# Kernel tuning notes

Measured on AMD Instinct MI355X. Metric: run time of the kernel, lower is better.

## Reference

```python
import jax, jax.numpy as jnp
import numpy as np

# dims per init_kwargs / input_specs
N, F_IN, H, C, L = 50000, 128, 128, 40, 4
E = 800000
ALPHA = 0.1   # args.beta -> self.alpha (initial-residual strength)
LAMDA = 0.5   # identity-mapping decay


def setup_inputs() -> dict:
    key = jax.random.key(0)
    ks = jax.random.split(key, 6)
    x = jax.random.normal(ks[0], (N, F_IN), jnp.float32)
    edge_index = jax.random.randint(ks[1], (2, E), 0, N, dtype=jnp.int32)
    s = 1.0 / np.sqrt(H)
    W_in = jax.random.uniform(ks[2], (F_IN, H), jnp.float32, -s, s)
    b_in = jnp.zeros((H,), jnp.float32)
    W_layers = jax.random.uniform(ks[3], (L, H, H), jnp.float32, -s, s)
    W_out = jax.random.uniform(ks[4], (H, C), jnp.float32, -s, s)
    b_out = jnp.zeros((C,), jnp.float32)
    return dict(x=x, edge_index=edge_index, W_in=W_in, b_in=b_in,
                W_layers=W_layers, W_out=W_out, b_out=b_out)


def _gcn_norm(edge_index, n):
    """Symmetric GCN normalization with added self-loops (gcn_norm)."""
    loops = jnp.arange(n, dtype=edge_index.dtype)
    row = jnp.concatenate([edge_index[0], loops])  # destination
    col = jnp.concatenate([edge_index[1], loops])  # source
    deg = jax.ops.segment_sum(jnp.ones(row.shape, jnp.float32), row, num_segments=n)
    dinv = jnp.where(deg > 0, jax.lax.rsqrt(jnp.maximum(deg, 1e-12)), 0.0)
    return row, col, dinv[row] * dinv[col]  # per-edge norm coefficient


def reference(x, edge_index, W_in, b_in, W_layers, W_out, b_out):
    n = x.shape[0]
    row, col, norm = _gcn_norm(edge_index, n)
    # input linear + relu (dropout is identity in eval / p=0)
    h = jax.nn.relu(x @ W_in + b_in)
    h0 = h  # _hidden[0], the initial residual
    # beta_i = log(lamda/(i+1) + 1)
    betas = jnp.log(LAMDA / jnp.arange(1, L + 1, dtype=jnp.float32) + 1.0)

    def layer(h, wb):
        W, beta = wb
        # sparse graph conv: gather-source, scale, scatter-add to dest  [E,H] msgs
        agg = jax.ops.segment_sum(h[col] * norm[:, None], row, num_segments=n)
        support = (1.0 - ALPHA) * agg + ALPHA * h0
        out = beta * (support @ W) + (1.0 - beta) * support  # ((1-b)I + bW)
        return jax.nn.relu(out), None

    h, _ = jax.lax.scan(layer, h, (W_layers, betas))
    return h @ W_out + b_out
```

## Files before the change

kernel.cpp:

```cpp
#include <hip/hip_runtime.h>
#include <hip/hip_bf16.h>
#include <hip/hip_fp16.h>
#include <math.h>

typedef short short8 __attribute__((ext_vector_type(8)));
typedef _Float16 half8 __attribute__((ext_vector_type(8)));
typedef float f32x4  __attribute__((ext_vector_type(4)));

__device__ __forceinline__ unsigned short f2bf(float f) {
    union { float f; unsigned u; } v; v.f = f;
    unsigned r = (v.u + 0x7FFFu + ((v.u >> 16) & 1u)) >> 16;
    return (unsigned short)r;
}
__device__ __forceinline__ float bf2f(unsigned short b) {
    union { unsigned u; float f; } v; v.u = ((unsigned)b) << 16; return v.f;
}
__device__ __forceinline__ unsigned short f2h(float f) {
    return __half_as_ushort(__float2half(f));
}
__device__ __forceinline__ float h2f(unsigned short u) {
    return __half2float(__ushort_as_half(u));
}


__global__ void k_count(const int* __restrict__ dst, int* __restrict__ cnt, int E) {
    int e = blockIdx.x * 256 + threadIdx.x;
    if (e < E) atomicAdd(&cnt[dst[e]], 1);
}

__global__ void k_dinv(const int* __restrict__ cnt, float* __restrict__ dinv, int n) {
    int i = blockIdx.x * 256 + threadIdx.x;
    if (i < n) dinv[i] = 1.0f / sqrtf((float)cnt[i] + 1.0f);
}

__global__ void k_scan_part(const int* __restrict__ cnt, int* __restrict__ offs,
                            int* __restrict__ parts, int n) {
    __shared__ int s[256];
    int i = blockIdx.x * 256 + threadIdx.x;
    int v = (i < n) ? cnt[i] : 0;
    s[threadIdx.x] = v;
    __syncthreads();
    #pragma unroll
    for (int d = 1; d < 256; d <<= 1) {
        int t = (threadIdx.x >= d) ? s[threadIdx.x - d] : 0;
        __syncthreads();
        s[threadIdx.x] += t;
        __syncthreads();
    }
    if (i < n) offs[i] = s[threadIdx.x] - v;
    if (threadIdx.x == 255) parts[blockIdx.x] = s[255];
}

__global__ void k_scan_tops(int* __restrict__ parts, int np) {
    __shared__ int s[256];
    int tid = threadIdx.x;
    int v = (tid < np) ? parts[tid] : 0;
    s[tid] = v;
    __syncthreads();
    #pragma unroll
    for (int d = 1; d < 256; d <<= 1) {
        int t = (tid >= d) ? s[tid - d] : 0;
        __syncthreads();
        s[tid] += t;
        __syncthreads();
    }
    if (tid < np) parts[tid] = s[tid] - v;
}

__global__ void k_scan_add(int* __restrict__ offs, const int* __restrict__ parts,
                           int n, int e_total) {
    int i = blockIdx.x * 256 + threadIdx.x;
    if (i < n) offs[i] += parts[blockIdx.x];
    if (blockIdx.x == 0 && threadIdx.x == 0) offs[n] = e_total;
}

__global__ void k_scatter(const int* __restrict__ dst, const int* __restrict__ src,
                          const int* __restrict__ offs, int* __restrict__ cur,
                          const float* __restrict__ dinv, unsigned* __restrict__ csr, int E) {
    int e = blockIdx.x * 256 + threadIdx.x;
    if (e < E) {
        int d = dst[e], s = src[e];
        int pos = offs[d] + atomicAdd(&cur[d], 1);
        float w = 0.9f * dinv[d] * dinv[s];
        unsigned hw = (unsigned)f2h(w);
        csr[pos] = (hw << 16) | (unsigned)s;
    }
}


__global__ void k_wprep(const float* __restrict__ Wl, const float* __restrict__ Win,
                        unsigned short* __restrict__ wt,
                        unsigned short* __restrict__ wht,
                        unsigned short* __restrict__ wlt) {
    int m = blockIdx.x;
    for (int i = threadIdx.x; i < 16384; i += 256) {
        int n = i >> 7, k = i & 127;
        if (m < 4) {
            wt[m * 16384 + n * 128 + k] = f2h(Wl[m * 16384 + k * 128 + n]);
        } else {
            float f = Win[k * 128 + n];
            unsigned short h = f2bf(f);
            wht[n * 128 + k] = h;
            wlt[n * 128 + k] = f2bf(f - bf2f(h));
        }
    }
}


__global__ __launch_bounds__(256)
void k_spmm(const int* __restrict__ offs, const unsigned* __restrict__ csr,
            const unsigned short* __restrict__ hb,
            const unsigned short* __restrict__ h0b,
            const float* __restrict__ dinv,
            unsigned short* __restrict__ supb, int n, int E) {
    int node = blockIdx.x * 8 + (threadIdx.x >> 5);
    if (node >= n) return;
    int l32 = threadIdx.x & 31;
    float di = dinv[node];
    float ws = 0.9f * di * di;
    uint2 sv = *(const uint2*)&hb [((size_t)node << 7) + (l32 << 2)];
    uint2 rv = *(const uint2*)&h0b[((size_t)node << 7) + (l32 << 2)];
    float ax = ws * h2f((unsigned short)(sv.x & 0xffffu)) + 0.1f * h2f((unsigned short)(rv.x & 0xffffu));
    float ay = ws * h2f((unsigned short)(sv.x >> 16))     + 0.1f * h2f((unsigned short)(rv.x >> 16));
    float az = ws * h2f((unsigned short)(sv.y & 0xffffu)) + 0.1f * h2f((unsigned short)(rv.y & 0xffffu));
    float aw = ws * h2f((unsigned short)(sv.y >> 16))     + 0.1f * h2f((unsigned short)(rv.y >> 16));
    int e = offs[node], end = offs[node + 1];
    while (e < end) {
        int nb = end - e;
        if (nb > 32) nb = 32;
        unsigned ce = csr[min(e + l32, E - 1)];
        int i = 0;
        for (; i + 8 <= nb; i += 8) {
            uint2 g[8]; float wv[8];
            #pragma unroll
            for (int j = 0; j < 8; ++j) {
                unsigned u = __shfl(ce, i + j, 32);
                wv[j] = h2f((unsigned short)(u >> 16));
                g[j] = *(const uint2*)&hb[((size_t)(u & 0xffffu) << 7) + (l32 << 2)];
            }
            #pragma unroll
            for (int j = 0; j < 8; ++j) {
                ax += wv[j] * h2f((unsigned short)(g[j].x & 0xffffu));
                ay += wv[j] * h2f((unsigned short)(g[j].x >> 16));
                az += wv[j] * h2f((unsigned short)(g[j].y & 0xffffu));
                aw += wv[j] * h2f((unsigned short)(g[j].y >> 16));
            }
        }
        for (; i + 4 <= nb; i += 4) {
            uint2 g[4]; float wv[4];
            #pragma unroll
            for (int j = 0; j < 4; ++j) {
                unsigned u = __shfl(ce, i + j, 32);
                wv[j] = h2f((unsigned short)(u >> 16));
                g[j] = *(const uint2*)&hb[((size_t)(u & 0xffffu) << 7) + (l32 << 2)];
            }
            #pragma unroll
            for (int j = 0; j < 4; ++j) {
                ax += wv[j] * h2f((unsigned short)(g[j].x & 0xffffu));
                ay += wv[j] * h2f((unsigned short)(g[j].x >> 16));
                az += wv[j] * h2f((unsigned short)(g[j].y & 0xffffu));
                aw += wv[j] * h2f((unsigned short)(g[j].y >> 16));
            }
        }
        for (; i + 2 <= nb; i += 2) {
            uint2 g[2]; float wv[2];
            #pragma unroll
            for (int j = 0; j < 2; ++j) {
                unsigned u = __shfl(ce, i + j, 32);
                wv[j] = h2f((unsigned short)(u >> 16));
                g[j] = *(const uint2*)&hb[((size_t)(u & 0xffffu) << 7) + (l32 << 2)];
            }
            #pragma unroll
            for (int j = 0; j < 2; ++j) {
                ax += wv[j] * h2f((unsigned short)(g[j].x & 0xffffu));
                ay += wv[j] * h2f((unsigned short)(g[j].x >> 16));
                az += wv[j] * h2f((unsigned short)(g[j].y & 0xffffu));
                aw += wv[j] * h2f((unsigned short)(g[j].y >> 16));
            }
        }
        for (; i < nb; ++i) {
            unsigned u = __shfl(ce, i, 32);
            float w = h2f((unsigned short)(u >> 16));
            uint2 g = *(const uint2*)&hb[((size_t)(u & 0xffffu) << 7) + (l32 << 2)];
            ax += w * h2f((unsigned short)(g.x & 0xffffu));
            ay += w * h2f((unsigned short)(g.x >> 16));
            az += w * h2f((unsigned short)(g.y & 0xffffu));
            aw += w * h2f((unsigned short)(g.y >> 16));
        }
        e += nb;
    }
    uint2 o;
    o.x = (unsigned)f2h(ax) | ((unsigned)f2h(ay) << 16);
    o.y = (unsigned)f2h(az) | ((unsigned)f2h(aw) << 16);
    *(uint2*)&supb[((size_t)node << 7) + (l32 << 2)] = o;
}


__global__ __launch_bounds__(256)
void gemm_in(const float* __restrict__ inA,
             const unsigned short* __restrict__ Bhi,
             const unsigned short* __restrict__ Blo,
             const float* __restrict__ bias,
             unsigned short* __restrict__ hb,
             unsigned short* __restrict__ h0b, int M) {
    extern __shared__ char lds[];
    char* Ahi = lds;
    char* Alo = Ahi + 8192;
    char* Whi = Alo + 8192;
    char* Wlo = Whi + 32768;

    const int tid  = threadIdx.x;
    const int row0 = blockIdx.x * 32;

    for (int c = tid; c < 512; c += 256) {
        int row = c >> 4, k8 = c & 15;
        int grow = row0 + row;
        short8 hv = {0,0,0,0,0,0,0,0};
        short8 lv = {0,0,0,0,0,0,0,0};
        if (grow < M) {
            const float* s = &inA[(size_t)grow * 128 + k8 * 8];
            float4 f0 = *(const float4*)s;
            float4 f1 = *(const float4*)(s + 4);
            float ff[8] = {f0.x, f0.y, f0.z, f0.w, f1.x, f1.y, f1.z, f1.w};
            #pragma unroll
            for (int j = 0; j < 8; ++j) {
                unsigned short hh = f2bf(ff[j]);
                hv[j] = (short)hh;
                lv[j] = (short)f2bf(ff[j] - bf2f(hh));
            }
        }
        int off = row * 256 + ((k8 ^ (row & 7)) << 4);
        *(short8*)(Ahi + off) = hv;
        *(short8*)(Alo + off) = lv;
    }
    for (int c = tid; c < 2048; c += 256) {
        int n = c >> 4, k8 = c & 15;
        int off = n * 256 + ((k8 ^ (n & 7)) << 4);
        *(short8*)(Whi + off) = *(const short8*)&Bhi[n * 128 + k8 * 8];
        *(short8*)(Wlo + off) = *(const short8*)&Blo[n * 128 + k8 * 8];
    }
    __syncthreads();

    const int lane = tid & 63;
    const int w    = tid >> 6;
    const int lr   = lane & 15;
    const int lg   = lane >> 4;

    f32x4 acc[2][2];
    #pragma unroll
    for (int m = 0; m < 2; ++m)
        #pragma unroll
        for (int n2 = 0; n2 < 2; ++n2) acc[m][n2] = (f32x4){0.f, 0.f, 0.f, 0.f};

    #pragma unroll
    for (int kk = 0; kk < 4; ++kk) {
        int k8 = kk * 4 + lg;
        short8 a[2], al[2], b[2], bl[2];
        #pragma unroll
        for (int m = 0; m < 2; ++m) {
            int row = m * 16 + lr;
            int off = row * 256 + ((k8 ^ (row & 7)) << 4);
            a[m]  = *(const short8*)(Ahi + off);
            al[m] = *(const short8*)(Alo + off);
        }
        #pragma unroll
        for (int n2 = 0; n2 < 2; ++n2) {
            int n = (w * 2 + n2) * 16 + lr;
            int off = n * 256 + ((k8 ^ (n & 7)) << 4);
            b[n2]  = *(const short8*)(Whi + off);
            bl[n2] = *(const short8*)(Wlo + off);
        }
        #pragma unroll
        for (int m = 0; m < 2; ++m)
            #pragma unroll
            for (int n2 = 0; n2 < 2; ++n2) {
                acc[m][n2] = __builtin_amdgcn_mfma_f32_16x16x32_bf16(al[m], b[n2], acc[m][n2], 0, 0, 0);
                acc[m][n2] = __builtin_amdgcn_mfma_f32_16x16x32_bf16(a[m], bl[n2], acc[m][n2], 0, 0, 0);
                acc[m][n2] = __builtin_amdgcn_mfma_f32_16x16x32_bf16(a[m], b[n2], acc[m][n2], 0, 0, 0);
            }
    }

    #pragma unroll
    for (int m = 0; m < 2; ++m) {
        #pragma unroll
        for (int n2 = 0; n2 < 2; ++n2) {
            int col = (w * 2 + n2) * 16 + lr;
            #pragma unroll
            for (int r = 0; r < 4; ++r) {
                int row = row0 + m * 16 + lg * 4 + r;
                if (row < M) {
                    float o = fmaxf(acc[m][n2][r] + bias[col], 0.f);
                    unsigned short ob = f2h(o);
                    hb [(size_t)row * 128 + col] = ob;
                    h0b[(size_t)row * 128 + col] = ob;
                }
            }
        }
    }
}


template<int LAST>
__global__ __launch_bounds__(256)
void gemm_layer(const unsigned short* __restrict__ supb,
                const unsigned short* __restrict__ Bh,
                float beta, float gamma,
                float* __restrict__ outf,
                unsigned short* __restrict__ outh, int M) {
    extern __shared__ char lds[];
    char* Ah = lds;
    char* Wh = Ah + 16384;

    const int tid  = threadIdx.x;
    const int row0 = blockIdx.x * 64;

    for (int c = tid; c < 1024; c += 256) {
        int row = c >> 4, k8 = c & 15;
        int grow = row0 + row;
        short8 hv = {0,0,0,0,0,0,0,0};
        if (grow < M) hv = *(const short8*)&supb[(size_t)grow * 128 + k8 * 8];
        *(short8*)(Ah + row * 256 + ((k8 ^ (row & 7)) << 4)) = hv;
    }
    for (int c = tid; c < 2048; c += 256) {
        int n = c >> 4, k8 = c & 15;
        *(short8*)(Wh + n * 256 + ((k8 ^ (n & 7)) << 4)) = *(const short8*)&Bh[n * 128 + k8 * 8];
    }
    __syncthreads();

    const int lane = tid & 63;
    const int w    = tid >> 6;
    const int lr   = lane & 15;
    const int lg   = lane >> 4;

    f32x4 acc[4][2];
    #pragma unroll
    for (int m = 0; m < 4; ++m)
        #pragma unroll
        for (int n2 = 0; n2 < 2; ++n2) acc[m][n2] = (f32x4){0.f, 0.f, 0.f, 0.f};

    #pragma unroll
    for (int kk = 0; kk < 4; ++kk) {
        int k8 = kk * 4 + lg;
        half8 a[4], b[2];
        #pragma unroll
        for (int m = 0; m < 4; ++m) {
            int row = m * 16 + lr;
            a[m] = *(const half8*)(Ah + row * 256 + ((k8 ^ (row & 7)) << 4));
        }
        #pragma unroll
        for (int n2 = 0; n2 < 2; ++n2) {
            int n = (w * 2 + n2) * 16 + lr;
            b[n2] = *(const half8*)(Wh + n * 256 + ((k8 ^ (n & 7)) << 4));
        }
        #pragma unroll
        for (int m = 0; m < 4; ++m)
            #pragma unroll
            for (int n2 = 0; n2 < 2; ++n2)
                acc[m][n2] = __builtin_amdgcn_mfma_f32_16x16x32_f16(a[m], b[n2], acc[m][n2], 0, 0, 0);
    }

    #pragma unroll
    for (int m = 0; m < 4; ++m) {
        #pragma unroll
        for (int n2 = 0; n2 < 2; ++n2) {
            int col = (w * 2 + n2) * 16 + lr;
            int k8c = col >> 3;
            int ebc = (col & 7) * 2;
            #pragma unroll
            for (int r = 0; r < 4; ++r) {
                int rl  = m * 16 + lg * 4 + r;
                int row = row0 + rl;
                if (row < M) {
                    unsigned short rb = *(const unsigned short*)
                        (Ah + rl * 256 + ((k8c ^ (rl & 7)) << 4) + ebc);
                    float o = beta * acc[m][n2][r] + gamma * h2f(rb);
                    o = fmaxf(o, 0.f);
                    if (LAST) outf[(size_t)row * 128 + col] = o;
                    else      outh[(size_t)row * 128 + col] = f2h(o);
                }
            }
        }
    }
}


__global__ __launch_bounds__(320)
void k_out(const float* __restrict__ h, const float* __restrict__ W,
           const float* __restrict__ b, float* __restrict__ out, int M, int C) {
    __shared__ float Ws[128 * 41];
    __shared__ float xs[32 * 132];
    const int tid  = threadIdx.x;
    const int row0 = blockIdx.x * 32;

    for (int i = tid; i < 128 * 40; i += 320) {
        int k = i / 40, c = i % 40;
        Ws[k * 41 + c] = W[i];
    }
    {
        const float4* h4 = (const float4*)h;
        for (int i = tid; i < 1024; i += 320) {
            int r = i >> 5, c4 = i & 31;
            int gr = row0 + r;
            float4 v = make_float4(0.f, 0.f, 0.f, 0.f);
            if (gr < M) v = h4[(size_t)gr * 32 + c4];
            *(float4*)&xs[r * 132 + c4 * 4] = v;
        }
    }
    __syncthreads();

    const int c  = tid % 40;
    const int rg = tid / 40;
    float acc[4] = {0.f, 0.f, 0.f, 0.f};
    #pragma unroll 4
    for (int k4 = 0; k4 < 32; ++k4) {
        float w0 = Ws[(k4 * 4 + 0) * 41 + c];
        float w1 = Ws[(k4 * 4 + 1) * 41 + c];
        float w2 = Ws[(k4 * 4 + 2) * 41 + c];
        float w3 = Ws[(k4 * 4 + 3) * 41 + c];
        #pragma unroll
        for (int i = 0; i < 4; ++i) {
            float4 x = *(const float4*)&xs[(rg * 4 + i) * 132 + k4 * 4];
            acc[i] += x.x * w0 + x.y * w1 + x.z * w2 + x.w * w3;
        }
    }
    float bb = b[c];
    #pragma unroll
    for (int i = 0; i < 4; ++i) {
        int r = row0 + rg * 4 + i;
        if (r < M) out[(size_t)r * C + c] = acc[i] + bb;
    }
}


extern "C" void kernel_launch(void* const* d_in, const int* in_sizes, int n_in,
                              void* d_out, int out_size, void* d_ws, size_t ws_size,
                              hipStream_t stream) {
    const float* x        = (const float*)d_in[0];
    const int*   ei       = (const int*)d_in[1];
    const float* W_in     = (const float*)d_in[2];
    const float* b_in     = (const float*)d_in[3];
    const float* W_layers = (const float*)d_in[4];
    const float* W_out    = (const float*)d_in[5];
    const float* b_out    = (const float*)d_in[6];
    float* out = (float*)d_out;

    const int H = 128;
    const int N = in_sizes[0] / H;
    const int E = in_sizes[1] / 2;
    const int L = in_sizes[4] / (H * H);
    const int C = in_sizes[5] / H;

    char* p = (char*)d_ws;
    auto alloc = [&](size_t bytes) {
        char* r = p;
        p += (bytes + 255) & ~(size_t)255;
        return r;
    };
    int*      cnt   = (int*)alloc((size_t)N * 4);
    int*      offs  = (int*)alloc((size_t)(N + 1) * 4);
    int*      parts = (int*)alloc(256 * 4);
    unsigned* csr   = (unsigned*)alloc((size_t)E * 4);
    float*    dinv  = (float*)alloc((size_t)N * 4);
    float*    hA    = (float*)alloc((size_t)N * H * 4);
    unsigned short* hb   = (unsigned short*)alloc((size_t)N * H * 2);
    unsigned short* h0b  = (unsigned short*)alloc((size_t)N * H * 2);
    unsigned short* supb = (unsigned short*)alloc((size_t)N * H * 2);
    unsigned short* wt   = (unsigned short*)alloc((size_t)L * H * H * 2);
    unsigned short* wht  = (unsigned short*)alloc((size_t)H * H * 2);
    unsigned short* wlt  = (unsigned short*)alloc((size_t)H * H * 2);
    (void)ws_size;

    const int* ei0 = ei;
    const int* ei1 = ei + E;

    const int nblkN = (N + 255) / 256;
    const int nblkE = (E + 255) / 256;

    k_wprep<<<5, 256, 0, stream>>>(W_layers, W_in, wt, wht, wlt);

    hipMemsetAsync(cnt, 0, (size_t)N * 4, stream);
    k_count<<<nblkE, 256, 0, stream>>>(ei0, cnt, E);
    k_dinv<<<nblkN, 256, 0, stream>>>(cnt, dinv, N);
    k_scan_part<<<nblkN, 256, 0, stream>>>(cnt, offs, parts, N);
    k_scan_tops<<<1, 256, 0, stream>>>(parts, nblkN);
    k_scan_add<<<nblkN, 256, 0, stream>>>(offs, parts, N, E);
    hipMemsetAsync(cnt, 0, (size_t)N * 4, stream);
    k_scatter<<<nblkE, 256, 0, stream>>>(ei0, ei1, offs, cnt, dinv, csr, E);

    gemm_in<<<(N + 31) / 32, 256, 80 * 1024, stream>>>(
        x, wht, wlt, b_in, hb, h0b, N);

    for (int l = 0; l < L; ++l) {
        float beta = logf(0.5f / (float)(l + 1) + 1.0f);
        k_spmm<<<(N + 7) / 8, 256, 0, stream>>>(offs, csr, hb, h0b, dinv, supb, N, E);
        if (l < L - 1)
            gemm_layer<0><<<(N + 63) / 64, 256, 48 * 1024, stream>>>(
                supb, wt + (size_t)l * H * H, beta, 1.0f - beta, nullptr, hb, N);
        else
            gemm_layer<1><<<(N + 63) / 64, 256, 48 * 1024, stream>>>(
                supb, wt + (size_t)l * H * H, beta, 1.0f - beta, hA, nullptr, N);
    }

    k_out<<<(N + 31) / 32, 320, 0, stream>>>(hA, W_out, b_out, out, N, C);
}
```

Baseline: 343.2 us.

## Use fp16 MFMA for input and output GEMMs and fuse preprocessing passes

Several changes land together. The input GEMM drops the split-bf16 three-MFMA emulation for a single fp16 MFMA with 64-row tiles. The output projection becomes an fp16 MFMA kernel that reads the fp16 hidden state, so the fp32 hidden buffer goes away. CSR construction records per-edge ranks during counting so the second memset and atomic pass are removed, the dinv computation is folded into the scan kernel, and the SpMM gains a 16-wide gather unroll. The gains should come from fewer MFMAs, fewer launches and less memory traffic, at the cost of lower precision in the input and output projections and a 16-bit rank that assumes in-degree stays below 65536.

```diff
diff --git a/kernel.cpp b/kernel.cpp
--- a/kernel.cpp
+++ b/kernel.cpp
@@ -7,14 +7,6 @@
 typedef _Float16 half8 __attribute__((ext_vector_type(8)));
 typedef float f32x4  __attribute__((ext_vector_type(4)));
 
-__device__ __forceinline__ unsigned short f2bf(float f) {
-    union { float f; unsigned u; } v; v.f = f;
-    unsigned r = (v.u + 0x7FFFu + ((v.u >> 16) & 1u)) >> 16;
-    return (unsigned short)r;
-}
-__device__ __forceinline__ float bf2f(unsigned short b) {
-    union { unsigned u; float f; } v; v.u = ((unsigned)b) << 16; return v.f;
-}
 __device__ __forceinline__ unsigned short f2h(float f) {
     return __half_as_ushort(__float2half(f));
 }
@@ -23,18 +15,14 @@
 }
 
 
-__global__ void k_count(const int* __restrict__ dst, int* __restrict__ cnt, int E) {
+__global__ void k_count(const int* __restrict__ dst, int* __restrict__ cnt,
+                        unsigned short* __restrict__ rank, int E) {
     int e = blockIdx.x * 256 + threadIdx.x;
-    if (e < E) atomicAdd(&cnt[dst[e]], 1);
-}
-
-__global__ void k_dinv(const int* __restrict__ cnt, float* __restrict__ dinv, int n) {
-    int i = blockIdx.x * 256 + threadIdx.x;
-    if (i < n) dinv[i] = 1.0f / sqrtf((float)cnt[i] + 1.0f);
+    if (e < E) rank[e] = (unsigned short)atomicAdd(&cnt[dst[e]], 1);
 }
 
 __global__ void k_scan_part(const int* __restrict__ cnt, int* __restrict__ offs,
-                            int* __restrict__ parts, int n) {
+                            int* __restrict__ parts, float* __restrict__ dinv, int n) {
     __shared__ int s[256];
     int i = blockIdx.x * 256 + threadIdx.x;
     int v = (i < n) ? cnt[i] : 0;
@@ -47,7 +35,10 @@
         s[threadIdx.x] += t;
         __syncthreads();
     }
-    if (i < n) offs[i] = s[threadIdx.x] - v;
+    if (i < n) {
+        offs[i] = s[threadIdx.x] - v;
+        dinv[i] = rsqrtf((float)v + 1.0f);
+    }
     if (threadIdx.x == 255) parts[blockIdx.x] = s[255];
 }
 
@@ -75,33 +66,39 @@
 }
 
 __global__ void k_scatter(const int* __restrict__ dst, const int* __restrict__ src,
-                          const int* __restrict__ offs, int* __restrict__ cur,
-                          const float* __restrict__ dinv, unsigned* __restrict__ csr, int E) {
+                          const unsigned short* __restrict__ rank,
+                          const int* __restrict__ offs,
+                          const float* __restrict__ dinv,
+                          unsigned* __restrict__ csr, int E) {
     int e = blockIdx.x * 256 + threadIdx.x;
     if (e < E) {
         int d = dst[e], s = src[e];
-        int pos = offs[d] + atomicAdd(&cur[d], 1);
         float w = 0.9f * dinv[d] * dinv[s];
-        unsigned hw = (unsigned)f2h(w);
-        csr[pos] = (hw << 16) | (unsigned)s;
+        csr[offs[d] + (int)rank[e]] = ((unsigned)f2h(w) << 16) | (unsigned)s;
     }
 }
 
 
 __global__ void k_wprep(const float* __restrict__ Wl, const float* __restrict__ Win,
+                        const float* __restrict__ Wout,
                         unsigned short* __restrict__ wt,
-                        unsigned short* __restrict__ wht,
-                        unsigned short* __restrict__ wlt) {
+                        unsigned short* __restrict__ wint,
+                        unsigned short* __restrict__ wot, int C) {
     int m = blockIdx.x;
-    for (int i = threadIdx.x; i < 16384; i += 256) {
-        int n = i >> 7, k = i & 127;
-        if (m < 4) {
+    if (m < 4) {
+        for (int i = threadIdx.x; i < 16384; i += 256) {
+            int n = i >> 7, k = i & 127;
             wt[m * 16384 + n * 128 + k] = f2h(Wl[m * 16384 + k * 128 + n]);
-        } else {
-            float f = Win[k * 128 + n];
-            unsigned short h = f2bf(f);
-            wht[n * 128 + k] = h;
-            wlt[n * 128 + k] = f2bf(f - bf2f(h));
+        }
+    } else if (m == 4) {
+        for (int i = threadIdx.x; i < 16384; i += 256) {
+            int n = i >> 7, k = i & 127;
+            wint[n * 128 + k] = f2h(Win[k * 128 + n]);
+        }
+    } else {
+        for (int i = threadIdx.x; i < 48 * 128; i += 256) {
+            int n = i >> 7, k = i & 127;
+            wot[n * 128 + k] = (n < C) ? f2h(Wout[k * C + n]) : (unsigned short)0;
         }
     }
 }
@@ -130,6 +127,22 @@
         if (nb > 32) nb = 32;
         unsigned ce = csr[min(e + l32, E - 1)];
         int i = 0;
+        for (; i + 16 <= nb; i += 16) {
+            uint2 g[16]; float wv[16];
+            #pragma unroll
+            for (int j = 0; j < 16; ++j) {
+                unsigned u = __shfl(ce, i + j, 32);
+                wv[j] = h2f((unsigned short)(u >> 16));
+                g[j] = *(const uint2*)&hb[((size_t)(u & 0xffffu) << 7) + (l32 << 2)];
+            }
+            #pragma unroll
+            for (int j = 0; j < 16; ++j) {
+                ax += wv[j] * h2f((unsigned short)(g[j].x & 0xffffu));
+                ay += wv[j] * h2f((unsigned short)(g[j].x >> 16));
+                az += wv[j] * h2f((unsigned short)(g[j].y & 0xffffu));
+                aw += wv[j] * h2f((unsigned short)(g[j].y >> 16));
+            }
+        }
         for (; i + 8 <= nb; i += 8) {
             uint2 g[8]; float wv[8];
             #pragma unroll
@@ -198,46 +211,34 @@
 
 __global__ __launch_bounds__(256)
 void gemm_in(const float* __restrict__ inA,
-             const unsigned short* __restrict__ Bhi,
-             const unsigned short* __restrict__ Blo,
+             const unsigned short* __restrict__ Bh,
              const float* __restrict__ bias,
              unsigned short* __restrict__ hb,
              unsigned short* __restrict__ h0b, int M) {
     extern __shared__ char lds[];
-    char* Ahi = lds;
-    char* Alo = Ahi + 8192;
-    char* Whi = Alo + 8192;
-    char* Wlo = Whi + 32768;
+    char* Ah = lds;
+    char* Wh = Ah + 16384;
 
     const int tid  = threadIdx.x;
-    const int row0 = blockIdx.x * 32;
-
-    for (int c = tid; c < 512; c += 256) {
+    const int row0 = blockIdx.x * 64;
+
+    for (int c = tid; c < 1024; c += 256) {
         int row = c >> 4, k8 = c & 15;
         int grow = row0 + row;
         short8 hv = {0,0,0,0,0,0,0,0};
-        short8 lv = {0,0,0,0,0,0,0,0};
         if (grow < M) {
             const float* s = &inA[(size_t)grow * 128 + k8 * 8];
             float4 f0 = *(const float4*)s;
             float4 f1 = *(const float4*)(s + 4);
             float ff[8] = {f0.x, f0.y, f0.z, f0.w, f1.x, f1.y, f1.z, f1.w};
             #pragma unroll
-            for (int j = 0; j < 8; ++j) {
-                unsigned short hh = f2bf(ff[j]);
-                hv[j] = (short)hh;
-                lv[j] = (short)f2bf(ff[j] - bf2f(hh));
-            }
-        }
-        int off = row * 256 + ((k8 ^ (row & 7)) << 4);
-        *(short8*)(Ahi + off) = hv;
-        *(short8*)(Alo + off) = lv;
+            for (int j = 0; j < 8; ++j) hv[j] = (short)f2h(ff[j]);
+        }
+        *(short8*)(Ah + row * 256 + ((k8 ^ (row & 7)) << 4)) = hv;
     }
     for (int c = tid; c < 2048; c += 256) {
         int n = c >> 4, k8 = c & 15;
-        int off = n * 256 + ((k8 ^ (n & 7)) << 4);
-        *(short8*)(Whi + off) = *(const short8*)&Bhi[n * 128 + k8 * 8];
-        *(short8*)(Wlo + off) = *(const short8*)&Blo[n * 128 + k8 * 8];
+        *(short8*)(Wh + n * 256 + ((k8 ^ (n & 7)) << 4)) = *(const short8*)&Bh[n * 128 + k8 * 8];
     }
     __syncthreads();
 
@@ -246,42 +247,35 @@
     const int lr   = lane & 15;
     const int lg   = lane >> 4;
 
-    f32x4 acc[2][2];
-    #pragma unroll
-    for (int m = 0; m < 2; ++m)
+    f32x4 acc[4][2];
+    #pragma unroll
+    for (int m = 0; m < 4; ++m)
         #pragma unroll
         for (int n2 = 0; n2 < 2; ++n2) acc[m][n2] = (f32x4){0.f, 0.f, 0.f, 0.f};
 
     #pragma unroll
     for (int kk = 0; kk < 4; ++kk) {
         int k8 = kk * 4 + lg;
-        short8 a[2], al[2], b[2], bl[2];
-        #pragma unroll
-        for (int m = 0; m < 2; ++m) {
+        half8 a[4], b[2];
+        #pragma unroll
+        for (int m = 0; m < 4; ++m) {
             int row = m * 16 + lr;
-            int off = row * 256 + ((k8 ^ (row & 7)) << 4);
-            a[m]  = *(const short8*)(Ahi + off);
-            al[m] = *(const short8*)(Alo + off);
+            a[m] = *(const half8*)(Ah + row * 256 + ((k8 ^ (row & 7)) << 4));
         }
         #pragma unroll
         for (int n2 = 0; n2 < 2; ++n2) {
             int n = (w * 2 + n2) * 16 + lr;
-            int off = n * 256 + ((k8 ^ (n & 7)) << 4);
-            b[n2]  = *(const short8*)(Whi + off);
-            bl[n2] = *(const short8*)(Wlo + off);
-        }
-        #pragma unroll
-        for (int m = 0; m < 2; ++m)
-            #pragma unroll
-            for (int n2 = 0; n2 < 2; ++n2) {
-                acc[m][n2] = __builtin_amdgcn_mfma_f32_16x16x32_bf16(al[m], b[n2], acc[m][n2], 0, 0, 0);
-                acc[m][n2] = __builtin_amdgcn_mfma_f32_16x16x32_bf16(a[m], bl[n2], acc[m][n2], 0, 0, 0);
-                acc[m][n2] = __builtin_amdgcn_mfma_f32_16x16x32_bf16(a[m], b[n2], acc[m][n2], 0, 0, 0);
-            }
-    }
-
-    #pragma unroll
-    for (int m = 0; m < 2; ++m) {
+            b[n2] = *(const half8*)(Wh + n * 256 + ((k8 ^ (n & 7)) << 4));
+        }
+        #pragma unroll
+        for (int m = 0; m < 4; ++m)
+            #pragma unroll
+            for (int n2 = 0; n2 < 2; ++n2)
+                acc[m][n2] = __builtin_amdgcn_mfma_f32_16x16x32_f16(a[m], b[n2], acc[m][n2], 0, 0, 0);
+    }
+
+    #pragma unroll
+    for (int m = 0; m < 4; ++m) {
         #pragma unroll
         for (int n2 = 0; n2 < 2; ++n2) {
             int col = (w * 2 + n2) * 16 + lr;
@@ -300,12 +294,10 @@
 }
 
 
-template<int LAST>
 __global__ __launch_bounds__(256)
 void gemm_layer(const unsigned short* __restrict__ supb,
                 const unsigned short* __restrict__ Bh,
                 float beta, float gamma,
-                float* __restrict__ outf,
                 unsigned short* __restrict__ outh, int M) {
     extern __shared__ char lds[];
     char* Ah = lds;
@@ -375,8 +367,7 @@
                         (Ah + rl * 256 + ((k8c ^ (rl & 7)) << 4) + ebc);
                     float o = beta * acc[m][n2][r] + gamma * h2f(rb);
                     o = fmaxf(o, 0.f);
-                    if (LAST) outf[(size_t)row * 128 + col] = o;
-                    else      outh[(size_t)row * 128 + col] = f2h(o);
+                    outh[(size_t)row * 128 + col] = f2h(o);
                 }
             }
         }
@@ -384,50 +375,64 @@
 }
 
 
-__global__ __launch_bounds__(320)
-void k_out(const float* __restrict__ h, const float* __restrict__ W,
-           const float* __restrict__ b, float* __restrict__ out, int M, int C) {
-    __shared__ float Ws[128 * 41];
-    __shared__ float xs[32 * 132];
+__global__ __launch_bounds__(256)
+void k_out(const unsigned short* __restrict__ hb,
+           const unsigned short* __restrict__ Wot,
+           const float* __restrict__ bias,
+           float* __restrict__ out, int M, int C) {
+    extern __shared__ char lds[];
+    char* Ah = lds;
+    char* Wh = Ah + 16384;
+
     const int tid  = threadIdx.x;
-    const int row0 = blockIdx.x * 32;
-
-    for (int i = tid; i < 128 * 40; i += 320) {
-        int k = i / 40, c = i % 40;
-        Ws[k * 41 + c] = W[i];
-    }
-    {
-        const float4* h4 = (const float4*)h;
-        for (int i = tid; i < 1024; i += 320) {
-            int r = i >> 5, c4 = i & 31;
-            int gr = row0 + r;
-            float4 v = make_float4(0.f, 0.f, 0.f, 0.f);
-            if (gr < M) v = h4[(size_t)gr * 32 + c4];
-            *(float4*)&xs[r * 132 + c4 * 4] = v;
-        }
+    const int row0 = blockIdx.x * 64;
+
+    for (int c = tid; c < 1024; c += 256) {
+        int row = c >> 4, k8 = c & 15;
+        int grow = row0 + row;
+        short8 hv = {0,0,0,0,0,0,0,0};
+        if (grow < M) hv = *(const short8*)&hb[(size_t)grow * 128 + k8 * 8];
+        *(short8*)(Ah + row * 256 + ((k8 ^ (row & 7)) << 4)) = hv;
+    }
+    for (int c = tid; c < 768; c += 256) {
+        int n = c >> 4, k8 = c & 15;
+        *(short8*)(Wh + n * 256 + ((k8 ^ (n & 7)) << 4)) = *(const short8*)&Wot[n * 128 + k8 * 8];
     }
     __syncthreads();
 
-    const int c  = tid % 40;
-    const int rg = tid / 40;
-    float acc[4] = {0.f, 0.f, 0.f, 0.f};
-    #pragma unroll 4
-    for (int k4 = 0; k4 < 32; ++k4) {
-        float w0 = Ws[(k4 * 4 + 0) * 41 + c];
-        float w1 = Ws[(k4 * 4 + 1) * 41 + c];
-        float w2 = Ws[(k4 * 4 + 2) * 41 + c];
-        float w3 = Ws[(k4 * 4 + 3) * 41 + c];
-        #pragma unroll
-        for (int i = 0; i < 4; ++i) {
-            float4 x = *(const float4*)&xs[(rg * 4 + i) * 132 + k4 * 4];
-            acc[i] += x.x * w0 + x.y * w1 + x.z * w2 + x.w * w3;
-        }
-    }
-    float bb = b[c];
-    #pragma unroll
-    for (int i = 0; i < 4; ++i) {
-        int r = row0 + rg * 4 + i;
-        if (r < M) out[(size_t)r * C + c] = acc[i] + bb;
+    const int lane = tid & 63;
+    const int w    = tid >> 6;
+    const int lr   = lane & 15;
+    const int lg   = lane >> 4;
+
+    f32x4 acc[3];
+    #pragma unroll
+    for (int n2 = 0; n2 < 3; ++n2) acc[n2] = (f32x4){0.f, 0.f, 0.f, 0.f};
+
+    #pragma unroll
+    for (int kk = 0; kk < 4; ++kk) {
+        int k8 = kk * 4 + lg;
+        int row = w * 16 + lr;
+        half8 a = *(const half8*)(Ah + row * 256 + ((k8 ^ (row & 7)) << 4));
+        #pragma unroll
+        for (int n2 = 0; n2 < 3; ++n2) {
+            int n = n2 * 16 + lr;
+            half8 b = *(const half8*)(Wh + n * 256 + ((k8 ^ (n & 7)) << 4));
+            acc[n2] = __builtin_amdgcn_mfma_f32_16x16x32_f16(a, b, acc[n2], 0, 0, 0);
+        }
+    }
+
+    #pragma unroll
+    for (int n2 = 0; n2 < 3; ++n2) {
+        int col = n2 * 16 + lr;
+        if (col < C) {
+            float bb = bias[col];
+            #pragma unroll
+            for (int r = 0; r < 4; ++r) {
+                int row = row0 + w * 16 + lg * 4 + r;
+                if (row < M) out[(size_t)row * C + col] = acc[n2][r] + bb;
+            }
+        }
     }
 }
 
@@ -460,14 +465,14 @@
     int*      offs  = (int*)alloc((size_t)(N + 1) * 4);
     int*      parts = (int*)alloc(256 * 4);
     unsigned* csr   = (unsigned*)alloc((size_t)E * 4);
+    unsigned short* rank = (unsigned short*)alloc((size_t)E * 2);
     float*    dinv  = (float*)alloc((size_t)N * 4);
-    float*    hA    = (float*)alloc((size_t)N * H * 4);
     unsigned short* hb   = (unsigned short*)alloc((size_t)N * H * 2);
     unsigned short* h0b  = (unsigned short*)alloc((size_t)N * H * 2);
     unsigned short* supb = (unsigned short*)alloc((size_t)N * H * 2);
     unsigned short* wt   = (unsigned short*)alloc((size_t)L * H * H * 2);
-    unsigned short* wht  = (unsigned short*)alloc((size_t)H * H * 2);
-    unsigned short* wlt  = (unsigned short*)alloc((size_t)H * H * 2);
+    unsigned short* wint = (unsigned short*)alloc((size_t)H * H * 2);
+    unsigned short* wot  = (unsigned short*)alloc((size_t)48 * H * 2);
     (void)ws_size;
 
     const int* ei0 = ei;
@@ -476,30 +481,23 @@
     const int nblkN = (N + 255) / 256;
     const int nblkE = (E + 255) / 256;
 
-    k_wprep<<<5, 256, 0, stream>>>(W_layers, W_in, wt, wht, wlt);
+    k_wprep<<<6, 256, 0, stream>>>(W_layers, W_in, W_out, wt, wint, wot, C);
 
     hipMemsetAsync(cnt, 0, (size_t)N * 4, stream);
-    k_count<<<nblkE, 256, 0, stream>>>(ei0, cnt, E);
-    k_dinv<<<nblkN, 256, 0, stream>>>(cnt, dinv, N);
-    k_scan_part<<<nblkN, 256, 0, stream>>>(cnt, offs, parts, N);
+    k_count<<<nblkE, 256, 0, stream>>>(ei0, cnt, rank, E);
+    k_scan_part<<<nblkN, 256, 0, stream>>>(cnt, offs, parts, dinv, N);
     k_scan_tops<<<1, 256, 0, stream>>>(parts, nblkN);
     k_scan_add<<<nblkN, 256, 0, stream>>>(offs, parts, N, E);
-    hipMemsetAsync(cnt, 0, (size_t)N * 4, stream);
-    k_scatter<<<nblkE, 256, 0, stream>>>(ei0, ei1, offs, cnt, dinv, csr, E);
-
-    gemm_in<<<(N + 31) / 32, 256, 80 * 1024, stream>>>(
-        x, wht, wlt, b_in, hb, h0b, N);
+    k_scatter<<<nblkE, 256, 0, stream>>>(ei0, ei1, rank, offs, dinv, csr, E);
+
+    gemm_in<<<(N + 63) / 64, 256, 48 * 1024, stream>>>(x, wint, b_in, hb, h0b, N);
 
     for (int l = 0; l < L; ++l) {
         float beta = logf(0.5f / (float)(l + 1) + 1.0f);
         k_spmm<<<(N + 7) / 8, 256, 0, stream>>>(offs, csr, hb, h0b, dinv, supb, N, E);
-        if (l < L - 1)
-            gemm_layer<0><<<(N + 63) / 64, 256, 48 * 1024, stream>>>(
-                supb, wt + (size_t)l * H * H, beta, 1.0f - beta, nullptr, hb, N);
-        else
-            gemm_layer<1><<<(N + 63) / 64, 256, 48 * 1024, stream>>>(
-                supb, wt + (size_t)l * H * H, beta, 1.0f - beta, hA, nullptr, N);
-    }
-
-    k_out<<<(N + 31) / 32, 320, 0, stream>>>(hA, W_out, b_out, out, N, C);
-}
+        gemm_layer<<<(N + 63) / 64, 256, 48 * 1024, stream>>>(
+            supb, wt + (size_t)l * H * H, beta, 1.0f - beta, hb, N);
+    }
+
+    k_out<<<(N + 63) / 64, 256, 28 * 1024, stream>>>(hb, wot, b_out, out, N, C);
+}
```

Result: faster. 294.5 us (-14.2%).
